# Performance work log

Hardware: AMD Instinct MI355X
Metric: run time of the kernel (lower is better)

Reference implementation:

```python
import jax, jax.numpy as jnp
import numpy as np

B, F, V, D_EMB = 16384, 32, 50000, 16
D_IN = F * D_EMB            # 512, concat embedding dim
N_TASK, N_SPEC, N_SH = 2, 2, 2
E = N_TASK * N_SPEC + N_SH  # 6 experts per CGC level
H1, H2 = 512, 256           # expert_params dims
T1, T2 = 128, 64            # tower dims


def setup_inputs() -> dict:
    key = jax.random.key(0)
    ks = iter(jax.random.split(key, 32))
    def w(shape, s=0.05):
        return jax.random.normal(next(ks), shape, jnp.float32) * s
    return dict(
        x_ids=jax.random.randint(next(ks), (B, F), 0, V),
        emb=w((F, V, D_EMB)),
        e1_W1=w((E, D_IN, H1)), e1_b1=jnp.zeros((E, H1), jnp.float32),
        e1_W2=w((E, H1, H2)), e1_b2=jnp.zeros((E, H2), jnp.float32),
        g1_Ws=w((N_TASK, D_IN, N_SPEC + N_SH)), g1_bs=jnp.zeros((N_TASK, N_SPEC + N_SH), jnp.float32),
        g1_Wsh=w((D_IN, E)), g1_bsh=jnp.zeros((E,), jnp.float32),
        e2_W1=w((E, H2, H1)), e2_b1=jnp.zeros((E, H1), jnp.float32),
        e2_W2=w((E, H1, H2)), e2_b2=jnp.zeros((E, H2), jnp.float32),
        g2_Ws=w((N_TASK, H2, N_SPEC + N_SH)), g2_bs=jnp.zeros((N_TASK, N_SPEC + N_SH), jnp.float32),
        tw_W1=w((N_TASK, H2, T1)), tw_b1=jnp.zeros((N_TASK, T1), jnp.float32),
        tw_W2=w((N_TASK, T1, T2)), tw_b2=jnp.zeros((N_TASK, T2), jnp.float32),
    )


def _cgc(x_list, W1, b1, W2, b2, Wg, bg, Wg_sh=None, bg_sh=None):
    # Stack expert inputs: task-t specific experts read x_list[t], shared read x_list[-1].
    X = jnp.stack([x_list[0]] * N_SPEC + [x_list[1]] * N_SPEC + [x_list[-1]] * N_SH)  # [E,B,Din]
    # Grouped two-layer expert MLP (BatchNorm is identity at eval-mode init).
    h = jax.nn.relu(jnp.einsum('ebd,edh->ebh', X, W1) + b1[:, None, :])   # [E,B,H1]
    out = jax.nn.relu(jnp.einsum('ebh,eho->ebo', h, W2) + b2[:, None, :])  # [E,B,H2]
    outs = []
    for t in range(N_TASK):
        gate = jax.nn.softmax(x_list[t] @ Wg[t] + bg[t], axis=-1)          # [B, N_SPEC+N_SH]
        sel = jnp.concatenate([out[t * N_SPEC:(t + 1) * N_SPEC], out[-N_SH:]], axis=0)
        outs.append(jnp.einsum('bk,kbo->bo', gate, sel))
    if Wg_sh is not None:  # shared gate only for levels < n_level
        gate = jax.nn.softmax(x_list[-1] @ Wg_sh + bg_sh, axis=-1)          # [B,E]
        outs.append(jnp.einsum('bk,kbo->bo', gate, out))
    return outs


def reference(x_ids, emb, e1_W1, e1_b1, e1_W2, e1_b2, g1_Ws, g1_bs, g1_Wsh, g1_bsh,
              e2_W1, e2_b1, e2_W2, e2_b2, g2_Ws, g2_bs, tw_W1, tw_b1, tw_W2, tw_b2):
    # Embedding lookup per sparse feature, then flatten (squeeze_dim=True).
    embed_x = emb[jnp.arange(F)[None, :], x_ids].reshape(B, D_IN)  # [B, 512]
    xs = [embed_x] * (N_TASK + 1)
    xs = _cgc(xs, e1_W1, e1_b1, e1_W2, e1_b2, g1_Ws, g1_bs, g1_Wsh, g1_bsh)  # level 1 -> 3 outs
    xs = _cgc(xs, e2_W1, e2_b1, e2_W2, e2_b2, g2_Ws, g2_bs)                  # level 2 -> 2 outs
    ys = []
    for t in range(N_TASK):
        h = jax.nn.relu(xs[t] @ tw_W1[t] + tw_b1[t])
        h = jax.nn.relu(h @ tw_W2[t] + tw_b2[t])
        ys.append(jax.nn.sigmoid(h))  # PredictionLayer('classification')
    return jnp.concatenate(ys, axis=1)  # [B, N_TASK*T2]
```

## Files before the change

### kernel.cpp

```cpp
#include <hip/hip_runtime.h>

typedef unsigned short u16;
typedef __attribute__((ext_vector_type(4))) unsigned short u16x4;
typedef __attribute__((ext_vector_type(8))) unsigned short u16x8;
typedef __attribute__((ext_vector_type(8))) short s16x8;
typedef __attribute__((ext_vector_type(4))) float f32x4;

#define BATCH 16384
#define NFEAT 32
#define NVOCAB 50000

__device__ __forceinline__ u16 f2bf(float f) {
    union { float f; unsigned u; } v; v.f = f;
    unsigned u = v.u;
    return (u16)((u + 0x7fffu + ((u >> 16) & 1u)) >> 16);
}
__device__ __forceinline__ float bf2f(u16 h) {
    union { unsigned u; float f; } v; v.u = ((unsigned)h) << 16;
    return v.f;
}

__device__ __forceinline__ void load_lds16(const u16* g, u16* l) {
    __builtin_amdgcn_global_load_lds(
        (const __attribute__((address_space(1))) void*)g,
        (__attribute__((address_space(3))) void*)l, 16, 0, 0);
}

struct PrepDesc { const float* src; u16* dst; int K; int N; int nz; int zbase; };
struct PrepArgs { PrepDesc d[6]; };

__global__ void prep_weights(PrepArgs args) {
    int z = blockIdx.z;
    int di = 0;
    #pragma unroll
    for (int i = 0; i < 6; i++)
        if (z >= args.d[i].zbase && z < args.d[i].zbase + args.d[i].nz) di = i;
    PrepDesc d = args.d[di];
    int zz = z - d.zbase;
    int k0 = blockIdx.x * 32, n0 = blockIdx.y * 32;
    if (k0 >= d.K || n0 >= d.N) return;
    __shared__ float tile[32][33];
    const float* src = d.src + (long)zz * d.K * d.N;
    u16* dst = d.dst + (long)zz * d.K * d.N;
    int tx = threadIdx.x & 31, ty = threadIdx.x >> 5;
    for (int r = ty; r < 32; r += 8) {
        int k = k0 + r, n = n0 + tx;
        tile[r][tx] = (k < d.K && n < d.N) ? src[(long)k * d.N + n] : 0.f;
    }
    __syncthreads();
    for (int r = ty; r < 32; r += 8) {
        int n = n0 + r, k = k0 + tx;
        if (n < d.N && k < d.K) dst[(long)n * d.K + k] = f2bf(tile[tx][r]);
    }
}

__global__ void gather_embed(const int* __restrict__ ids,
                             const float* __restrict__ emb,
                             u16* __restrict__ out) {
    int idx = blockIdx.x * 256 + threadIdx.x;
    int d4 = idx & 3;
    int f  = (idx >> 2) & 31;
    int b  = idx >> 7;
    int id = ids[b * NFEAT + f];
    const float4* p = (const float4*)(emb + ((long)f * NVOCAB + id) * 16) + d4;
    float4 v = *p;
    u16x4 o;
    o.x = f2bf(v.x); o.y = f2bf(v.y); o.z = f2bf(v.z); o.w = f2bf(v.w);
    *(u16x4*)(out + (long)b * 512 + f * 16 + d4 * 4) = o;
}

struct FusedP {
    const u16* A; const u16* W1t; const float* b1;
    const u16* W2t; const float* b2; u16* O;
    int K1, a_zshift; long a_zstride;
};

__device__ __forceinline__ void expert_impl(const FusedP p) {
    __shared__ u16 sA[64 * 64];
    __shared__ u16 sW[256 * 64];
    __shared__ u16 sH[64 * 128];
    const int z = blockIdx.z;
    const int m0 = blockIdx.x * 64;
    const u16* Ab  = p.A + (long)(z >> p.a_zshift) * p.a_zstride;
    const u16* W1b = p.W1t + (long)z * 512 * p.K1;
    const u16* W2b = p.W2t + (long)z * 256 * 512;
    const int K1 = p.K1;
    const int tid = threadIdx.x;
    const int lane = tid & 63;
    const int w = tid >> 6;
    const int l16 = lane & 15;
    const int q = lane >> 4;
    const int key = l16 & 7;

    const int tr = tid >> 3;
    const int lc = (tid & 7) ^ (tr & 7);
    const u16* gA0 = Ab + (long)(m0 + tr) * K1 + lc * 8;
    const int ldst = (tid & ~63) * 8;

    f32x4 acc[4][4] = {};

    #pragma unroll
    for (int c = 0; c < 4; c++) {
        f32x4 acc1[4][2] = {};
        for (int k0 = 0; k0 < K1; k0 += 64) {
            __syncthreads();
            #pragma unroll
            for (int i = 0; i < 2; i++)
                load_lds16(gA0 + (long)(32 * i) * K1 + k0, &sA[i * 2048 + ldst]);
            #pragma unroll
            for (int i = 0; i < 4; i++)
                load_lds16(W1b + (long)(c * 128 + 32 * i + tr) * K1 + k0 + lc * 8,
                           &sW[i * 2048 + ldst]);
            __syncthreads();
            #pragma unroll
            for (int kk = 0; kk < 2; kk++) {
                const int pc = ((kk << 2) | q) ^ key;
                s16x8 af[4], bf[2];
                #pragma unroll
                for (int mt = 0; mt < 4; mt++)
                    af[mt] = *(const s16x8*)(&sA[(mt * 16 + l16) * 64 + pc * 8]);
                #pragma unroll
                for (int nt = 0; nt < 2; nt++)
                    bf[nt] = *(const s16x8*)(&sW[(w * 32 + nt * 16 + l16) * 64 + pc * 8]);
                #pragma unroll
                for (int mt = 0; mt < 4; mt++)
                    #pragma unroll
                    for (int nt = 0; nt < 2; nt++)
                        acc1[mt][nt] = __builtin_amdgcn_mfma_f32_16x16x32_bf16(
                            bf[nt], af[mt], acc1[mt][nt], 0, 0, 0);
            }
        }
        __syncthreads();
        {
            const float* bb1 = p.b1 + (long)z * 512 + c * 128;
            #pragma unroll
            for (int mt = 0; mt < 4; mt++) {
                int r = mt * 16 + l16;
                #pragma unroll
                for (int nt = 0; nt < 2; nt++) {
                    int col = w * 32 + nt * 16 + q * 4;
                    float4 bv = *(const float4*)(bb1 + col);
                    f32x4 v = acc1[mt][nt];
                    u16x4 o;
                    o.x = f2bf(fmaxf(v.x + bv.x, 0.f));
                    o.y = f2bf(fmaxf(v.y + bv.y, 0.f));
                    o.z = f2bf(fmaxf(v.z + bv.z, 0.f));
                    o.w = f2bf(fmaxf(v.w + bv.w, 0.f));
                    int c8 = col >> 3;
                    *(u16x4*)(&sH[r * 128 + ((c8 ^ (r & 7)) << 3) + (q & 1) * 4]) = o;
                }
            }
        }
        #pragma unroll
        for (int s = 0; s < 2; s++) {
            __syncthreads();
            #pragma unroll
            for (int i = 0; i < 8; i++)
                load_lds16(W2b + (long)(32 * i + tr) * 512 + c * 128 + s * 64 + lc * 8,
                           &sW[i * 2048 + ldst]);
            __syncthreads();
            #pragma unroll
            for (int kk = 0; kk < 2; kk++) {
                const int kg = s * 8 + ((kk << 2) | q);
                const int pc = ((kk << 2) | q) ^ key;
                s16x8 af[4], bf[4];
                #pragma unroll
                for (int mt = 0; mt < 4; mt++) {
                    int r = mt * 16 + l16;
                    af[mt] = *(const s16x8*)(&sH[r * 128 + ((kg ^ key) << 3)]);
                }
                #pragma unroll
                for (int nt = 0; nt < 4; nt++)
                    bf[nt] = *(const s16x8*)(&sW[(w * 64 + nt * 16 + l16) * 64 + pc * 8]);
                #pragma unroll
                for (int mt = 0; mt < 4; mt++)
                    #pragma unroll
                    for (int nt = 0; nt < 4; nt++)
                        acc[mt][nt] = __builtin_amdgcn_mfma_f32_16x16x32_bf16(
                            bf[nt], af[mt], acc[mt][nt], 0, 0, 0);
            }
        }
    }

    const float* bb2 = p.b2 + (long)z * 256;
    u16* Op = p.O + (long)z * BATCH * 256;
    #pragma unroll
    for (int mt = 0; mt < 4; mt++) {
        int grow = m0 + mt * 16 + l16;
        u16* rowp = Op + (long)grow * 256;
        #pragma unroll
        for (int nt = 0; nt < 4; nt++) {
            int gc = w * 64 + nt * 16 + q * 4;
            float4 bv = *(const float4*)(bb2 + gc);
            f32x4 v = acc[mt][nt];
            v.x = fmaxf(v.x + bv.x, 0.f);
            v.y = fmaxf(v.y + bv.y, 0.f);
            v.z = fmaxf(v.z + bv.z, 0.f);
            v.w = fmaxf(v.w + bv.w, 0.f);
            u16x4 o;
            o.x = f2bf(v.x); o.y = f2bf(v.y); o.z = f2bf(v.z); o.w = f2bf(v.w);
            *(u16x4*)(rowp + gc) = o;
        }
    }
}

__global__ __launch_bounds__(256, 2) void fused_l1(FusedP p) { expert_impl(p); }
__global__ __launch_bounds__(256, 2) void fused_l2(FusedP p) { expert_impl(p); }

__global__ __launch_bounds__(256, 1)
void tower_fused(const u16* __restrict__ x2, const u16* __restrict__ W1t,
                 const float* __restrict__ b1, const u16* __restrict__ W2t,
                 const float* __restrict__ b2, float* __restrict__ out) {
    const int t = blockIdx.y, m0 = blockIdx.x * 64;
    __shared__ u16 sX[64 * 256];
    __shared__ u16 sW1[128 * 256];
    __shared__ u16 sH[64 * 136];
    __shared__ u16 sW2[64 * 128];
    __shared__ float sB1[128];
    __shared__ float sB2[64];
    const int tid = threadIdx.x, lane = tid & 63, w = tid >> 6;
    const int l16 = lane & 15, q = lane >> 4;

    #pragma unroll
    for (int i = 0; i < 8; i++) {
        int c = i * 256 + tid, row = c >> 5, kc = c & 31;
        int lcc = (kc & ~7) | ((kc & 7) ^ (row & 7));
        load_lds16(x2 + ((long)t * BATCH + m0 + row) * 256 + lcc * 8,
                   &sX[(i * 256 + (tid & ~63)) * 8]);
    }
    #pragma unroll
    for (int i = 0; i < 16; i++) {
        int c = i * 256 + tid, row = c >> 5, kc = c & 31;
        int lcc = (kc & ~7) | ((kc & 7) ^ (row & 7));
        load_lds16(W1t + ((long)t * 128 + row) * 256 + lcc * 8,
                   &sW1[(i * 256 + (tid & ~63)) * 8]);
    }
    #pragma unroll
    for (int i = 0; i < 4; i++) {
        int c = i * 256 + tid, row = c >> 4, kc = c & 15;
        int lcc = (kc & ~7) | ((kc & 7) ^ (row & 7));
        load_lds16(W2t + ((long)t * 64 + row) * 128 + lcc * 8,
                   &sW2[(i * 256 + (tid & ~63)) * 8]);
    }
    if (tid < 128) sB1[tid] = b1[t * 128 + tid];
    if (tid < 64)  sB2[tid] = b2[t * 64 + tid];
    __syncthreads();

    f32x4 acc1[4][2] = {};
    #pragma unroll
    for (int kk = 0; kk < 8; kk++) {
        int pcb = kk * 4 + q;
        s16x8 af[4], bf[2];
        #pragma unroll
        for (int mt = 0; mt < 4; mt++) {
            int row = mt * 16 + l16;
            int sc = (pcb & ~7) | ((pcb & 7) ^ (row & 7));
            af[mt] = *(const s16x8*)(&sX[row * 256 + sc * 8]);
        }
        #pragma unroll
        for (int nt = 0; nt < 2; nt++) {
            int row = w * 32 + nt * 16 + l16;
            int sc = (pcb & ~7) | ((pcb & 7) ^ (row & 7));
            bf[nt] = *(const s16x8*)(&sW1[row * 256 + sc * 8]);
        }
        #pragma unroll
        for (int mt = 0; mt < 4; mt++)
            #pragma unroll
            for (int nt = 0; nt < 2; nt++)
                acc1[mt][nt] = __builtin_amdgcn_mfma_f32_16x16x32_bf16(
                    bf[nt], af[mt], acc1[mt][nt], 0, 0, 0);
    }
    #pragma unroll
    for (int mt = 0; mt < 4; mt++) {
        int row = mt * 16 + l16;
        #pragma unroll
        for (int nt = 0; nt < 2; nt++) {
            int col = w * 32 + nt * 16 + q * 4;
            f32x4 v = acc1[mt][nt];
            u16x4 o;
            o.x = f2bf(fmaxf(v.x + sB1[col + 0], 0.f));
            o.y = f2bf(fmaxf(v.y + sB1[col + 1], 0.f));
            o.z = f2bf(fmaxf(v.z + sB1[col + 2], 0.f));
            o.w = f2bf(fmaxf(v.w + sB1[col + 3], 0.f));
            *(u16x4*)(&sH[row * 136 + col]) = o;
        }
    }
    __syncthreads();

    f32x4 acc2[4] = {};
    #pragma unroll
    for (int kk = 0; kk < 4; kk++) {
        s16x8 af[4], bf;
        #pragma unroll
        for (int mt = 0; mt < 4; mt++) {
            int row = mt * 16 + l16;
            af[mt] = *(const s16x8*)(&sH[row * 136 + kk * 32 + q * 8]);
        }
        {
            int row = w * 16 + l16;
            int pc = kk * 4 + q;
            int sc = (pc & ~7) | ((pc & 7) ^ (row & 7));
            bf = *(const s16x8*)(&sW2[row * 128 + sc * 8]);
        }
        #pragma unroll
        for (int mt = 0; mt < 4; mt++)
            acc2[mt] = __builtin_amdgcn_mfma_f32_16x16x32_bf16(
                bf, af[mt], acc2[mt], 0, 0, 0);
    }
    #pragma unroll
    for (int mt = 0; mt < 4; mt++) {
        int grow = m0 + mt * 16 + l16;
        int col = w * 16 + q * 4;
        float4 bv = *(const float4*)(sB2 + col);
        f32x4 v = acc2[mt];
        float4 r;
        r.x = 1.f / (1.f + __expf(-(v.x + bv.x)));
        r.y = 1.f / (1.f + __expf(-(v.y + bv.y)));
        r.z = 1.f / (1.f + __expf(-(v.z + bv.z)));
        r.w = 1.f / (1.f + __expf(-(v.w + bv.w)));
        *(float4*)(out + (long)grow * 128 + t * 64 + col) = r;
    }
}

__global__ __launch_bounds__(256)
void gate1(const u16* __restrict__ embed, const u16* __restrict__ out1,
           const float* __restrict__ g1Ws, const float* __restrict__ g1bs,
           const float* __restrict__ gWsh, const float* __restrict__ gbsh,
           u16* __restrict__ x1) {
    const int m0 = blockIdx.x * 8;
    __shared__ float sg[8][16];
    const int tid = threadIdx.x;
    const int row = tid >> 5, l = tid & 31;
    const long rb = m0 + row;

    float a[4] = {0,0,0,0}, b[4] = {0,0,0,0}, c[6] = {0,0,0,0,0,0};
    {
        const u16* er = embed + rb * 512 + l * 16;
        u16x8 xa = *(const u16x8*)(er);
        u16x8 xb = *(const u16x8*)(er + 8);
        #pragma unroll
        for (int u = 0; u < 16; u++) {
            int k = l * 16 + u;
            float xv = bf2f(u < 8 ? xa[u] : xb[u - 8]);
            float4 wa = *(const float4*)(g1Ws + k * 4);
            float4 wb = *(const float4*)(g1Ws + 2048 + k * 4);
            a[0] += xv * wa.x; a[1] += xv * wa.y; a[2] += xv * wa.z; a[3] += xv * wa.w;
            b[0] += xv * wb.x; b[1] += xv * wb.y; b[2] += xv * wb.z; b[3] += xv * wb.w;
            float2 w0 = *(const float2*)(gWsh + k * 6);
            float2 w1 = *(const float2*)(gWsh + k * 6 + 2);
            float2 w2 = *(const float2*)(gWsh + k * 6 + 4);
            c[0] += xv * w0.x; c[1] += xv * w0.y;
            c[2] += xv * w1.x; c[3] += xv * w1.y;
            c[4] += xv * w2.x; c[5] += xv * w2.y;
        }
    }
    #pragma unroll
    for (int off = 1; off < 32; off <<= 1) {
        #pragma unroll
        for (int g = 0; g < 4; g++) { a[g] += __shfl_xor(a[g], off); b[g] += __shfl_xor(b[g], off); }
        #pragma unroll
        for (int g = 0; g < 6; g++) c[g] += __shfl_xor(c[g], off);
    }
    if (l == 0) {
        float mx, s, e[6];
        mx = -1e30f;
        for (int g = 0; g < 4; g++) { a[g] += g1bs[g]; mx = fmaxf(mx, a[g]); }
        s = 0.f; for (int g = 0; g < 4; g++) { e[g] = __expf(a[g] - mx); s += e[g]; }
        for (int g = 0; g < 4; g++) sg[row][g] = e[g] / s;
        mx = -1e30f;
        for (int g = 0; g < 4; g++) { b[g] += g1bs[4 + g]; mx = fmaxf(mx, b[g]); }
        s = 0.f; for (int g = 0; g < 4; g++) { e[g] = __expf(b[g] - mx); s += e[g]; }
        for (int g = 0; g < 4; g++) sg[row][4 + g] = e[g] / s;
        mx = -1e30f;
        for (int g = 0; g < 6; g++) { c[g] += gbsh[g]; mx = fmaxf(mx, c[g]); }
        s = 0.f; for (int g = 0; g < 6; g++) { e[g] = __expf(c[g] - mx); s += e[g]; }
        for (int g = 0; g < 6; g++) sg[row][8 + g] = e[g] / s;
    }
    __syncthreads();

    const int c8 = l * 8;
    const u16* ob = out1 + rb * 256 + c8;
    u16x8 o[6];
    #pragma unroll
    for (int k = 0; k < 6; k++) o[k] = *(const u16x8*)(ob + (long)k * BATCH * 256);
    const float* g = sg[row];
    u16x8 r0, r1, r2;
    #pragma unroll
    for (int u = 0; u < 8; u++) {
        float o0 = bf2f(o[0][u]), o1 = bf2f(o[1][u]), o2 = bf2f(o[2][u]);
        float o3 = bf2f(o[3][u]), o4 = bf2f(o[4][u]), o5 = bf2f(o[5][u]);
        r0[u] = f2bf(g[0] * o0 + g[1] * o1 + g[2] * o4 + g[3] * o5);
        r1[u] = f2bf(g[4] * o2 + g[5] * o3 + g[6] * o4 + g[7] * o5);
        r2[u] = f2bf(g[8] * o0 + g[9] * o1 + g[10] * o2 + g[11] * o3 + g[12] * o4 + g[13] * o5);
    }
    *(u16x8*)(x1 + ((long)0 * BATCH + rb) * 256 + c8) = r0;
    *(u16x8*)(x1 + ((long)1 * BATCH + rb) * 256 + c8) = r1;
    *(u16x8*)(x1 + ((long)2 * BATCH + rb) * 256 + c8) = r2;
}

__global__ __launch_bounds__(256)
void gate2(const u16* __restrict__ x1, const u16* __restrict__ out2,
           const float* __restrict__ g2Ws, const float* __restrict__ g2bs,
           u16* __restrict__ x2) {
    const int m0 = blockIdx.x * 8;
    __shared__ float sg[8][8];
    const int tid = threadIdx.x;
    const int row = tid >> 5, l = tid & 31;
    const long rb = m0 + row;

    float a[4] = {0,0,0,0}, b[4] = {0,0,0,0};
    {
        const u16* e0 = x1 + rb * 256 + l * 8;
        const u16* e1 = e0 + (long)BATCH * 256;
        u16x8 x0 = *(const u16x8*)e0;
        u16x8 x1v = *(const u16x8*)e1;
        #pragma unroll
        for (int u = 0; u < 8; u++) {
            int k = l * 8 + u;
            float4 wa = *(const float4*)(g2Ws + k * 4);
            float4 wb = *(const float4*)(g2Ws + 1024 + k * 4);
            float xv0 = bf2f(x0[u]), xv1 = bf2f(x1v[u]);
            a[0] += xv0 * wa.x; a[1] += xv0 * wa.y; a[2] += xv0 * wa.z; a[3] += xv0 * wa.w;
            b[0] += xv1 * wb.x; b[1] += xv1 * wb.y; b[2] += xv1 * wb.z; b[3] += xv1 * wb.w;
        }
    }
    #pragma unroll
    for (int off = 1; off < 32; off <<= 1) {
        #pragma unroll
        for (int g = 0; g < 4; g++) { a[g] += __shfl_xor(a[g], off); b[g] += __shfl_xor(b[g], off); }
    }
    if (l == 0) {
        float mx, s, e[4];
        mx = -1e30f;
        for (int g = 0; g < 4; g++) { a[g] += g2bs[g]; mx = fmaxf(mx, a[g]); }
        s = 0.f; for (int g = 0; g < 4; g++) { e[g] = __expf(a[g] - mx); s += e[g]; }
        for (int g = 0; g < 4; g++) sg[row][g] = e[g] / s;
        mx = -1e30f;
        for (int g = 0; g < 4; g++) { b[g] += g2bs[4 + g]; mx = fmaxf(mx, b[g]); }
        s = 0.f; for (int g = 0; g < 4; g++) { e[g] = __expf(b[g] - mx); s += e[g]; }
        for (int g = 0; g < 4; g++) sg[row][4 + g] = e[g] / s;
    }
    __syncthreads();

    const int c8 = l * 8;
    const u16* ob = out2 + rb * 256 + c8;
    u16x8 o[6];
    #pragma unroll
    for (int k = 0; k < 6; k++) o[k] = *(const u16x8*)(ob + (long)k * BATCH * 256);
    const float* g = sg[row];
    u16x8 r0, r1;
    #pragma unroll
    for (int u = 0; u < 8; u++) {
        float o0 = bf2f(o[0][u]), o1 = bf2f(o[1][u]), o2 = bf2f(o[2][u]);
        float o3 = bf2f(o[3][u]), o4 = bf2f(o[4][u]), o5 = bf2f(o[5][u]);
        r0[u] = f2bf(g[0] * o0 + g[1] * o1 + g[2] * o4 + g[3] * o5);
        r1[u] = f2bf(g[4] * o2 + g[5] * o3 + g[6] * o4 + g[7] * o5);
    }
    *(u16x8*)(x2 + ((long)0 * BATCH + rb) * 256 + c8) = r0;
    *(u16x8*)(x2 + ((long)1 * BATCH + rb) * 256 + c8) = r1;
}

extern "C" void kernel_launch(void* const* d_in, const int* in_sizes, int n_in,
                              void* d_out, int out_size, void* d_ws, size_t ws_size,
                              hipStream_t stream) {
    const int*   x_ids = (const int*)  d_in[0];
    const float* emb   = (const float*)d_in[1];
    const float* e1W1  = (const float*)d_in[2];
    const float* e1b1  = (const float*)d_in[3];
    const float* e1W2  = (const float*)d_in[4];
    const float* e1b2  = (const float*)d_in[5];
    const float* g1Ws  = (const float*)d_in[6];
    const float* g1bs  = (const float*)d_in[7];
    const float* g1Wsh = (const float*)d_in[8];
    const float* g1bsh = (const float*)d_in[9];
    const float* e2W1  = (const float*)d_in[10];
    const float* e2b1  = (const float*)d_in[11];
    const float* e2W2  = (const float*)d_in[12];
    const float* e2b2  = (const float*)d_in[13];
    const float* g2Ws  = (const float*)d_in[14];
    const float* g2bs  = (const float*)d_in[15];
    const float* twW1  = (const float*)d_in[16];
    const float* twb1  = (const float*)d_in[17];
    const float* twW2  = (const float*)d_in[18];
    const float* twb2  = (const float*)d_in[19];
    float* out = (float*)d_out;

    char* ws = (char*)d_ws;
    u16* embed   = (u16*)(ws + 0);
    u16* wt_e1W1 = (u16*)(ws + 16777216);
    u16* wt_e1W2 = (u16*)(ws + 19922944);
    u16* wt_e2W1 = (u16*)(ws + 21495808);
    u16* wt_e2W2 = (u16*)(ws + 23068672);
    u16* wt_twW1 = (u16*)(ws + 24641536);
    u16* wt_twW2 = (u16*)(ws + 24772608);
    u16* o_buf   = (u16*)(ws + 125468672);
    u16* x1      = (u16*)(ws + 175800320);
    u16* x2      = (u16*)(ws + 200966144);

    PrepArgs pa;
    pa.d[0] = { e1W1, wt_e1W1, 512, 512, 6,  0 };
    pa.d[1] = { e1W2, wt_e1W2, 512, 256, 6,  6 };
    pa.d[2] = { e2W1, wt_e2W1, 256, 512, 6, 12 };
    pa.d[3] = { e2W2, wt_e2W2, 512, 256, 6, 18 };
    pa.d[4] = { twW1, wt_twW1, 256, 128, 2, 24 };
    pa.d[5] = { twW2, wt_twW2, 128,  64, 2, 26 };
    prep_weights<<<dim3(16, 16, 28), 256, 0, stream>>>(pa);

    gather_embed<<<dim3(BATCH * NFEAT * 4 / 256), 256, 0, stream>>>(x_ids, emb, embed);

    FusedP f1 = { embed, wt_e1W1, e1b1, wt_e1W2, e1b2, o_buf, 512, 3, 0L };
    fused_l1<<<dim3(BATCH / 64, 1, 6), 256, 0, stream>>>(f1);

    gate1<<<dim3(BATCH / 8), 256, 0, stream>>>(embed, o_buf, g1Ws, g1bs, g1Wsh, g1bsh, x1);

    FusedP f2 = { x1, wt_e2W1, e2b1, wt_e2W2, e2b2, o_buf, 256, 1, (long)BATCH * 256 };
    fused_l2<<<dim3(BATCH / 64, 1, 6), 256, 0, stream>>>(f2);

    gate2<<<dim3(BATCH / 8), 256, 0, stream>>>(x1, o_buf, g2Ws, g2bs, x2);

    tower_fused<<<dim3(BATCH / 64, 2), 256, 0, stream>>>(x2, wt_twW1, twb1, wt_twW2, twb2, out);
}
```

Measured before the change: 507.2 us.

## Split level-1 expert MLP into two pipelined large-tile GEMMs

```diff
diff --git a/kernel.cpp b/kernel.cpp
--- a/kernel.cpp
+++ b/kernel.cpp
@@ -68,6 +68,146 @@
     o.x = f2bf(v.x); o.y = f2bf(v.y); o.z = f2bf(v.z); o.w = f2bf(v.w);
     *(u16x4*)(out + (long)b * 512 + f * 16 + d4 * 4) = o;
 }
+
+struct GemmP {
+    const u16* A; const u16* Bt; const float* bias; u16* C;
+    int N, K, a_zshift, c_row_stride; long a_zstride, c_zstride;
+};
+
+__device__ __forceinline__ void gemm8_impl(const GemmP p) {
+    __shared__ u16 sA[3][128 * 64];
+    __shared__ u16 sB[3][256 * 64];
+    const int z = blockIdx.z;
+    const u16* Ab = p.A + (long)(z >> p.a_zshift) * p.a_zstride;
+    const u16* Bb = p.Bt + (long)z * p.N * p.K;
+    const int m0 = blockIdx.x * 128;
+    const int n0 = blockIdx.y * 256;
+    const int tid = threadIdx.x;
+    const int lane = tid & 63;
+    const int w = tid >> 6;
+    const int wm = (w >> 2) * 64;
+    const int wn = (w & 3) * 64;
+    const int l16 = lane & 15;
+    const int q = lane >> 4;
+    const int key = l16 & 7;
+    const int K = p.K;
+    const int NT = K >> 6;
+
+    const int tr = tid >> 3;
+    const int lc = (tid & 7) ^ (tr & 7);
+    const u16* gA0 = Ab + (long)(m0 + tr) * K + lc * 8;
+    const u16* gB0 = Bb + (long)(n0 + tr) * K + lc * 8;
+    const int ldst = (tid & ~63) * 8;
+
+    f32x4 acc[4][4] = {};
+
+    #pragma unroll
+    for (int i = 0; i < 2; i++) load_lds16(gA0 + (long)(64 * i) * K,      &sA[0][ldst + i * 4096]);
+    #pragma unroll
+    for (int i = 0; i < 4; i++) load_lds16(gB0 + (long)(64 * i) * K,      &sB[0][ldst + i * 4096]);
+    #pragma unroll
+    for (int i = 0; i < 2; i++) load_lds16(gA0 + (long)(64 * i) * K + 64, &sA[1][ldst + i * 4096]);
+    #pragma unroll
+    for (int i = 0; i < 4; i++) load_lds16(gB0 + (long)(64 * i) * K + 64, &sB[1][ldst + i * 4096]);
+
+    int cb = 0;
+    for (int t = 0; t < NT; ++t) {
+        int pb = cb + 2; if (pb >= 3) pb -= 3;
+
+        if (t + 1 < NT) asm volatile("s_waitcnt vmcnt(6)" ::: "memory");
+        else            asm volatile("s_waitcnt vmcnt(0)" ::: "memory");
+        __builtin_amdgcn_s_barrier();
+        __builtin_amdgcn_sched_barrier(0);
+
+        const u16* A_ = sA[cb];
+        const u16* B_ = sB[cb];
+        u16* Ap = sA[pb];
+        u16* Bp = sB[pb];
+        const bool pf = (t + 2) < NT;
+        const int kpf = (t + 2) << 6;
+
+        {
+            s16x8 af[4], bf[4];
+            #pragma unroll
+            for (int mt = 0; mt < 4; mt++)
+                af[mt] = *(const s16x8*)(&A_[(wm + mt * 16 + l16) * 64 + ((q ^ key) * 8)]);
+            #pragma unroll
+            for (int nt = 0; nt < 4; nt++)
+                bf[nt] = *(const s16x8*)(&B_[(wn + nt * 16 + l16) * 64 + ((q ^ key) * 8)]);
+            if (pf) {
+                load_lds16(gA0 + (long)kpf,          &Ap[ldst]);
+                load_lds16(gA0 + (long)64 * K + kpf, &Ap[ldst + 4096]);
+                load_lds16(gB0 + (long)kpf,          &Bp[ldst]);
+            }
+            __builtin_amdgcn_sched_barrier(0);
+            __builtin_amdgcn_s_barrier();
+            asm volatile("s_waitcnt lgkmcnt(0)" ::: "memory");
+            __builtin_amdgcn_sched_barrier(0);
+            __builtin_amdgcn_s_setprio(1);
+            #pragma unroll
+            for (int mt = 0; mt < 4; mt++)
+                #pragma unroll
+                for (int nt = 0; nt < 4; nt++)
+                    acc[mt][nt] = __builtin_amdgcn_mfma_f32_16x16x32_bf16(
+                        bf[nt], af[mt], acc[mt][nt], 0, 0, 0);
+            __builtin_amdgcn_s_setprio(0);
+        }
+        __builtin_amdgcn_s_barrier();
+        __builtin_amdgcn_sched_barrier(0);
+
+        {
+            s16x8 af[4], bf[4];
+            #pragma unroll
+            for (int mt = 0; mt < 4; mt++)
+                af[mt] = *(const s16x8*)(&A_[(wm + mt * 16 + l16) * 64 + (((4 | q) ^ key) * 8)]);
+            #pragma unroll
+            for (int nt = 0; nt < 4; nt++)
+                bf[nt] = *(const s16x8*)(&B_[(wn + nt * 16 + l16) * 64 + (((4 | q) ^ key) * 8)]);
+            if (pf) {
+                load_lds16(gB0 + (long)64 * K + kpf,  &Bp[ldst + 4096]);
+                load_lds16(gB0 + (long)128 * K + kpf, &Bp[ldst + 2 * 4096]);
+                load_lds16(gB0 + (long)192 * K + kpf, &Bp[ldst + 3 * 4096]);
+            }
+            __builtin_amdgcn_sched_barrier(0);
+            __builtin_amdgcn_s_barrier();
+            asm volatile("s_waitcnt lgkmcnt(0)" ::: "memory");
+            __builtin_amdgcn_sched_barrier(0);
+            __builtin_amdgcn_s_setprio(1);
+            #pragma unroll
+            for (int mt = 0; mt < 4; mt++)
+                #pragma unroll
+                for (int nt = 0; nt < 4; nt++)
+                    acc[mt][nt] = __builtin_amdgcn_mfma_f32_16x16x32_bf16(
+                        bf[nt], af[mt], acc[mt][nt], 0, 0, 0);
+            __builtin_amdgcn_s_setprio(0);
+        }
+        cb = cb + 1; if (cb >= 3) cb = 0;
+    }
+
+    const float* bb = p.bias + (long)z * p.N;
+    u16* Cp = p.C + (long)z * p.c_zstride;
+    #pragma unroll
+    for (int mt = 0; mt < 4; mt++) {
+        int grow = m0 + wm + mt * 16 + l16;
+        u16* rowp = Cp + (long)grow * p.c_row_stride;
+        #pragma unroll
+        for (int nt = 0; nt < 4; nt++) {
+            int gc = n0 + wn + nt * 16 + q * 4;
+            float4 bv = *(const float4*)(bb + gc);
+            f32x4 v = acc[mt][nt];
+            v.x = fmaxf(v.x + bv.x, 0.f);
+            v.y = fmaxf(v.y + bv.y, 0.f);
+            v.z = fmaxf(v.z + bv.z, 0.f);
+            v.w = fmaxf(v.w + bv.w, 0.f);
+            u16x4 o;
+            o.x = f2bf(v.x); o.y = f2bf(v.y); o.z = f2bf(v.z); o.w = f2bf(v.w);
+            *(u16x4*)(rowp + gc) = o;
+        }
+    }
+}
+
+__global__ __launch_bounds__(512, 2) void gemm_l1a(GemmP p) { gemm8_impl(p); }
+__global__ __launch_bounds__(512, 2) void gemm_l1b(GemmP p) { gemm8_impl(p); }
 
 struct FusedP {
     const u16* A; const u16* W1t; const float* b1;
@@ -204,7 +344,6 @@
     }
 }
 
-__global__ __launch_bounds__(256, 2) void fused_l1(FusedP p) { expert_impl(p); }
 __global__ __launch_bounds__(256, 2) void fused_l2(FusedP p) { expert_impl(p); }
 
 __global__ __launch_bounds__(256, 1)
@@ -493,6 +632,7 @@
     u16* wt_e2W2 = (u16*)(ws + 23068672);
     u16* wt_twW1 = (u16*)(ws + 24641536);
     u16* wt_twW2 = (u16*)(ws + 24772608);
+    u16* h_buf   = (u16*)(ws + 24805376);
     u16* o_buf   = (u16*)(ws + 125468672);
     u16* x1      = (u16*)(ws + 175800320);
     u16* x2      = (u16*)(ws + 200966144);
@@ -508,8 +648,12 @@
 
     gather_embed<<<dim3(BATCH * NFEAT * 4 / 256), 256, 0, stream>>>(x_ids, emb, embed);
 
-    FusedP f1 = { embed, wt_e1W1, e1b1, wt_e1W2, e1b2, o_buf, 512, 3, 0L };
-    fused_l1<<<dim3(BATCH / 64, 1, 6), 256, 0, stream>>>(f1);
+    GemmP p1a = { embed, wt_e1W1, e1b1, h_buf, 512, 512, 0, 512, 0L, (long)BATCH * 512 };
+    gemm_l1a<<<dim3(128, 2, 6), 512, 0, stream>>>(p1a);
+
+    GemmP p1b = { h_buf, wt_e1W2, e1b2, o_buf, 256, 512, 0, 256,
+                  (long)BATCH * 512, (long)BATCH * 256 };
+    gemm_l1b<<<dim3(128, 1, 6), 512, 0, stream>>>(p1b);
 
     gate1<<<dim3(BATCH / 8), 256, 0, stream>>>(embed, o_buf, g1Ws, g1bs, g1Wsh, g1bsh, x1);
 
```

New measurement: 529.1 us. +4.3%, slower.

## Read expert weights directly from global in MFMA fragment layout, stage full A tile once

Applied to the files above, without the earlier changes.

```diff
diff --git a/kernel.cpp b/kernel.cpp
--- a/kernel.cpp
+++ b/kernel.cpp
@@ -26,7 +26,7 @@
         (__attribute__((address_space(3))) void*)l, 16, 0, 0);
 }
 
-struct PrepDesc { const float* src; u16* dst; int K; int N; int nz; int zbase; };
+struct PrepDesc { const float* src; u16* dst; int K; int N; int nz; int zbase; int frag; };
 struct PrepArgs { PrepDesc d[6]; };
 
 __global__ void prep_weights(PrepArgs args) {
@@ -50,7 +50,16 @@
     __syncthreads();
     for (int r = ty; r < 32; r += 8) {
         int n = n0 + r, k = k0 + tx;
-        if (n < d.N && k < d.K) dst[(long)n * d.K + k] = f2bf(tile[tx][r]);
+        if (n < d.N && k < d.K) {
+            u16 v = f2bf(tile[tx][r]);
+            if (d.frag) {
+                long idx = (((long)(n >> 4) * (d.K >> 5) + (k >> 5)) * 4 + ((k >> 3) & 3)) * 128
+                         + (long)(n & 15) * 8 + (k & 7);
+                dst[idx] = v;
+            } else {
+                dst[(long)n * d.K + k] = v;
+            }
+        }
     }
 }
 
@@ -70,21 +79,21 @@
 }
 
 struct FusedP {
-    const u16* A; const u16* W1t; const float* b1;
-    const u16* W2t; const float* b2; u16* O;
-    int K1, a_zshift; long a_zstride;
+    const u16* __restrict__ A; const u16* __restrict__ W1t; const float* __restrict__ b1;
+    const u16* __restrict__ W2t; const float* __restrict__ b2; u16* __restrict__ O;
+    int a_zshift; long a_zstride;
 };
 
+template<int NKT>
 __device__ __forceinline__ void expert_impl(const FusedP p) {
-    __shared__ u16 sA[64 * 64];
-    __shared__ u16 sW[256 * 64];
+    __shared__ u16 sA[64 * 64 * NKT];
     __shared__ u16 sH[64 * 128];
+    const int K1 = NKT * 64;
     const int z = blockIdx.z;
     const int m0 = blockIdx.x * 64;
     const u16* Ab  = p.A + (long)(z >> p.a_zshift) * p.a_zstride;
-    const u16* W1b = p.W1t + (long)z * 512 * p.K1;
-    const u16* W2b = p.W2t + (long)z * 256 * 512;
-    const int K1 = p.K1;
+    const u16* W1f = p.W1t + (long)z * 512 * K1;
+    const u16* W2f = p.W2t + (long)z * 256 * 512;
     const int tid = threadIdx.x;
     const int lane = tid & 63;
     const int w = tid >> 6;
@@ -92,40 +101,45 @@
     const int q = lane >> 4;
     const int key = l16 & 7;
 
+    const u16* W1l = W1f + q * 128 + l16 * 8;
+    const u16* W2l = W2f + q * 128 + l16 * 8;
+
     const int tr = tid >> 3;
     const int lc = (tid & 7) ^ (tr & 7);
     const u16* gA0 = Ab + (long)(m0 + tr) * K1 + lc * 8;
     const int ldst = (tid & ~63) * 8;
+    #pragma unroll
+    for (int kt = 0; kt < NKT; ++kt) {
+        #pragma unroll
+        for (int i = 0; i < 2; ++i)
+            load_lds16(gA0 + (long)(32 * i) * K1 + kt * 64, &sA[kt * 4096 + i * 2048 + ldst]);
+    }
+    __syncthreads();
 
     f32x4 acc[4][4] = {};
 
     #pragma unroll
-    for (int c = 0; c < 4; c++) {
+    for (int c = 0; c < 4; ++c) {
         f32x4 acc1[4][2] = {};
-        for (int k0 = 0; k0 < K1; k0 += 64) {
-            __syncthreads();
+        #pragma unroll 2
+        for (int kt = 0; kt < NKT; ++kt) {
             #pragma unroll
-            for (int i = 0; i < 2; i++)
-                load_lds16(gA0 + (long)(32 * i) * K1 + k0, &sA[i * 2048 + ldst]);
-            #pragma unroll
-            for (int i = 0; i < 4; i++)
-                load_lds16(W1b + (long)(c * 128 + 32 * i + tr) * K1 + k0 + lc * 8,
-                           &sW[i * 2048 + ldst]);
-            __syncthreads();
-            #pragma unroll
-            for (int kk = 0; kk < 2; kk++) {
+            for (int kk = 0; kk < 2; ++kk) {
                 const int pc = ((kk << 2) | q) ^ key;
                 s16x8 af[4], bf[2];
                 #pragma unroll
-                for (int mt = 0; mt < 4; mt++)
-                    af[mt] = *(const s16x8*)(&sA[(mt * 16 + l16) * 64 + pc * 8]);
-                #pragma unroll
-                for (int nt = 0; nt < 2; nt++)
-                    bf[nt] = *(const s16x8*)(&sW[(w * 32 + nt * 16 + l16) * 64 + pc * 8]);
-                #pragma unroll
-                for (int mt = 0; mt < 4; mt++)
+                for (int mt = 0; mt < 4; ++mt)
+                    af[mt] = *(const s16x8*)(&sA[kt * 4096 + (mt * 16 + l16) * 64 + pc * 8]);
+                #pragma unroll
+                for (int nt = 0; nt < 2; ++nt) {
+                    const int ntile = c * 8 + w * 2 + nt;
+                    const int ks = kt * 2 + kk;
+                    bf[nt] = *(const s16x8*)(W1l + (((long)ntile * (NKT * 2) + ks) << 9));
+                }
+                #pragma unroll
+                for (int mt = 0; mt < 4; ++mt)
                     #pragma unroll
-                    for (int nt = 0; nt < 2; nt++)
+                    for (int nt = 0; nt < 2; ++nt)
                         acc1[mt][nt] = __builtin_amdgcn_mfma_f32_16x16x32_bf16(
                             bf[nt], af[mt], acc1[mt][nt], 0, 0, 0);
             }
@@ -134,10 +148,10 @@
         {
             const float* bb1 = p.b1 + (long)z * 512 + c * 128;
             #pragma unroll
-            for (int mt = 0; mt < 4; mt++) {
+            for (int mt = 0; mt < 4; ++mt) {
                 int r = mt * 16 + l16;
                 #pragma unroll
-                for (int nt = 0; nt < 2; nt++) {
+                for (int nt = 0; nt < 2; ++nt) {
                     int col = w * 32 + nt * 16 + q * 4;
                     float4 bv = *(const float4*)(bb1 + col);
                     f32x4 v = acc1[mt][nt];
@@ -151,31 +165,28 @@
                 }
             }
         }
-        #pragma unroll
-        for (int s = 0; s < 2; s++) {
-            __syncthreads();
+        __syncthreads();
+        #pragma unroll
+        for (int s = 0; s < 2; ++s) {
             #pragma unroll
-            for (int i = 0; i < 8; i++)
-                load_lds16(W2b + (long)(32 * i + tr) * 512 + c * 128 + s * 64 + lc * 8,
-                           &sW[i * 2048 + ldst]);
-            __syncthreads();
-            #pragma unroll
-            for (int kk = 0; kk < 2; kk++) {
+            for (int kk = 0; kk < 2; ++kk) {
                 const int kg = s * 8 + ((kk << 2) | q);
-                const int pc = ((kk << 2) | q) ^ key;
                 s16x8 af[4], bf[4];
                 #pragma unroll
-                for (int mt = 0; mt < 4; mt++) {
+                for (int mt = 0; mt < 4; ++mt) {
                     int r = mt * 16 + l16;
                     af[mt] = *(const s16x8*)(&sH[r * 128 + ((kg ^ key) << 3)]);
                 }
                 #pragma unroll
-                for (int nt = 0; nt < 4; nt++)
-                    bf[nt] = *(const s16x8*)(&sW[(w * 64 + nt * 16 + l16) * 64 + pc * 8]);
-                #pragma unroll
-                for (int mt = 0; mt < 4; mt++)
+                for (int nt = 0; nt < 4; ++nt) {
+                    const int ntile = w * 4 + nt;
+                    const int ks2 = c * 4 + s * 2 + kk;
+                    bf[nt] = *(const s16x8*)(W2l + (((long)ntile * 16 + ks2) << 9));
+                }
+                #pragma unroll
+                for (int mt = 0; mt < 4; ++mt)
                     #pragma unroll
-                    for (int nt = 0; nt < 4; nt++)
+                    for (int nt = 0; nt < 4; ++nt)
                         acc[mt][nt] = __builtin_amdgcn_mfma_f32_16x16x32_bf16(
                             bf[nt], af[mt], acc[mt][nt], 0, 0, 0);
             }
@@ -185,11 +196,11 @@
     const float* bb2 = p.b2 + (long)z * 256;
     u16* Op = p.O + (long)z * BATCH * 256;
     #pragma unroll
-    for (int mt = 0; mt < 4; mt++) {
+    for (int mt = 0; mt < 4; ++mt) {
         int grow = m0 + mt * 16 + l16;
         u16* rowp = Op + (long)grow * 256;
         #pragma unroll
-        for (int nt = 0; nt < 4; nt++) {
+        for (int nt = 0; nt < 4; ++nt) {
             int gc = w * 64 + nt * 16 + q * 4;
             float4 bv = *(const float4*)(bb2 + gc);
             f32x4 v = acc[mt][nt];
@@ -204,8 +215,8 @@
     }
 }
 
-__global__ __launch_bounds__(256, 2) void fused_l1(FusedP p) { expert_impl(p); }
-__global__ __launch_bounds__(256, 2) void fused_l2(FusedP p) { expert_impl(p); }
+__global__ __launch_bounds__(256, 2) void fused_l1(FusedP p) { expert_impl<8>(p); }
+__global__ __launch_bounds__(256, 2) void fused_l2(FusedP p) { expert_impl<4>(p); }
 
 __global__ __launch_bounds__(256, 1)
 void tower_fused(const u16* __restrict__ x2, const u16* __restrict__ W1t,
@@ -498,22 +509,22 @@
     u16* x2      = (u16*)(ws + 200966144);
 
     PrepArgs pa;
-    pa.d[0] = { e1W1, wt_e1W1, 512, 512, 6,  0 };
-    pa.d[1] = { e1W2, wt_e1W2, 512, 256, 6,  6 };
-    pa.d[2] = { e2W1, wt_e2W1, 256, 512, 6, 12 };
-    pa.d[3] = { e2W2, wt_e2W2, 512, 256, 6, 18 };
-    pa.d[4] = { twW1, wt_twW1, 256, 128, 2, 24 };
-    pa.d[5] = { twW2, wt_twW2, 128,  64, 2, 26 };
+    pa.d[0] = { e1W1, wt_e1W1, 512, 512, 6,  0, 1 };
+    pa.d[1] = { e1W2, wt_e1W2, 512, 256, 6,  6, 1 };
+    pa.d[2] = { e2W1, wt_e2W1, 256, 512, 6, 12, 1 };
+    pa.d[3] = { e2W2, wt_e2W2, 512, 256, 6, 18, 1 };
+    pa.d[4] = { twW1, wt_twW1, 256, 128, 2, 24, 0 };
+    pa.d[5] = { twW2, wt_twW2, 128,  64, 2, 26, 0 };
     prep_weights<<<dim3(16, 16, 28), 256, 0, stream>>>(pa);
 
     gather_embed<<<dim3(BATCH * NFEAT * 4 / 256), 256, 0, stream>>>(x_ids, emb, embed);
 
-    FusedP f1 = { embed, wt_e1W1, e1b1, wt_e1W2, e1b2, o_buf, 512, 3, 0L };
+    FusedP f1 = { embed, wt_e1W1, e1b1, wt_e1W2, e1b2, o_buf, 3, 0L };
     fused_l1<<<dim3(BATCH / 64, 1, 6), 256, 0, stream>>>(f1);
 
     gate1<<<dim3(BATCH / 8), 256, 0, stream>>>(embed, o_buf, g1Ws, g1bs, g1Wsh, g1bsh, x1);
 
-    FusedP f2 = { x1, wt_e2W1, e2b1, wt_e2W2, e2b2, o_buf, 256, 1, (long)BATCH * 256 };
+    FusedP f2 = { x1, wt_e2W1, e2b1, wt_e2W2, e2b2, o_buf, 1, (long)BATCH * 256 };
     fused_l2<<<dim3(BATCH / 64, 1, 6), 256, 0, stream>>>(f2);
 
     gate2<<<dim3(BATCH / 8), 256, 0, stream>>>(x1, o_buf, g2Ws, g2bs, x2);
```

New measurement: 562.5 us. 1.11x slower.
